# Kernel optimization log

Hardware: AMD Instinct MI355X
Metric: run time of the kernel (lower is better)

The kernel has to match this reference:

```python
import jax, jax.numpy as jnp
import numpy as np

N_HEAD = 16


def setup_inputs() -> dict:
    key = jax.random.key(0)
    k1, k2, k3 = jax.random.split(key, 3)
    B, T, C = 2, 2048, 1024
    x = jax.random.normal(k1, (B, T, C), dtype=jnp.float32)
    attention_mask = jnp.zeros((B, 1, 1, T), dtype=jnp.float32)
    W_attn = jax.random.normal(k2, (C, 3 * C), dtype=jnp.float32) * 0.02
    b_attn = jnp.zeros((3 * C,), dtype=jnp.float32)
    W_proj = jax.random.normal(k3, (C, C), dtype=jnp.float32) * 0.02
    b_proj = jnp.zeros((C,), dtype=jnp.float32)
    return {"x": x, "attention_mask": attention_mask, "W_attn": W_attn,
            "b_attn": b_attn, "W_proj": W_proj, "b_proj": b_proj}


def reference(x, attention_mask, W_attn, b_attn, W_proj, b_proj):
    B, T, C = x.shape
    H = N_HEAD
    d = C // H
    qkv = x @ W_attn + b_attn                      # [B, T, 3C]
    q, k, v = jnp.split(qkv, 3, axis=-1)
    q = q.reshape(B, T, H, d).transpose(0, 2, 1, 3)  # [B, H, T, d]
    k = k.reshape(B, T, H, d).transpose(0, 2, 1, 3)
    v = v.reshape(B, T, H, d).transpose(0, 2, 1, 3)
    att = jnp.einsum('bhtd,bhsd->bhts', q, k) * (1.0 / np.sqrt(d))
    causal = jnp.tril(jnp.ones((T, T), dtype=bool))
    att = jnp.where(causal[None, None], att, jnp.float32(-10000.0))
    att = att + attention_mask                     # additive broadcast mask
    att = jax.nn.softmax(att, axis=-1)             # dropout p=0.0 -> identity
    y = jnp.einsum('bhts,bhsd->bhtd', att, v)      # [B, H, T, d]
    y = y.transpose(0, 2, 1, 3).reshape(B, T, C)
    return y @ W_proj + b_proj
```

## Files before the change

kernel.cpp:

```cpp
#include <hip/hip_runtime.h>
#include <hip/hip_bf16.h>
#include <stdint.h>

#define BATCH 2
#define TT 2048
#define CC 1024
#define NH 16
#define HD 64

typedef __attribute__((ext_vector_type(8))) short short8;
typedef __attribute__((ext_vector_type(4))) short sh4;
typedef __attribute__((ext_vector_type(4))) float f32x4;
typedef __attribute__((ext_vector_type(2))) unsigned uint2v;

#define MFMA16 __builtin_amdgcn_mfma_f32_16x16x32_bf16

#define LOG2E 1.4426950408889634f

#if defined(__has_builtin)
#if __has_builtin(__builtin_amdgcn_exp2f)
#define EXP2(x) __builtin_amdgcn_exp2f(x)
#else
#define EXP2(x) __expf((x) * 0.6931471805599453f)
#endif
#else
#define EXP2(x) __expf((x) * 0.6931471805599453f)
#endif

__device__ __forceinline__ short f2bf(float f) {
  union { float f; unsigned u; } x;
  x.f = f;
  unsigned r = x.u + 0x7FFFu + ((x.u >> 16) & 1u);
  return (short)(r >> 16);
}

__device__ __forceinline__ void transpose_cast_tile(
    const float* __restrict__ W, short* __restrict__ Wt, int K, int N,
    int n0, int k0, int tid) {
  __shared__ __align__(16) float Ls[64][68];
  {
    const int r = tid >> 4, c4 = (tid & 15) * 4;
#pragma unroll
    for (int p = 0; p < 4; ++p) {
      const float4 v = *reinterpret_cast<const float4*>(
          &W[(size_t)(k0 + r + p * 16) * N + n0 + c4]);
      *reinterpret_cast<float4*>(&Ls[r + p * 16][c4]) = v;
    }
  }
  __syncthreads();
  {
    const int n = tid >> 2;
    const int kk0 = (tid & 3) * 16;
#pragma unroll
    for (int half = 0; half < 2; ++half) {
      short8 o;
#pragma unroll
      for (int t = 0; t < 8; ++t) o[t] = f2bf(Ls[kk0 + half * 8 + t][n]);
      *reinterpret_cast<short8*>(&Wt[(size_t)(n0 + n) * K + k0 + kk0 + half * 8]) = o;
    }
  }
}

__global__ __launch_bounds__(256) void prep_fused(
    const float* __restrict__ x, short* __restrict__ xb,
    const float* __restrict__ W_attn, short* __restrict__ wat,
    const float* __restrict__ W_proj, short* __restrict__ wpt) {
  const int blk = blockIdx.x;
  const int tid = threadIdx.x;
  if (blk < 2048) {
    const int i = (blk * 256 + tid) * 8;
    const float4 a = *reinterpret_cast<const float4*>(&x[i]);
    const float4 b = *reinterpret_cast<const float4*>(&x[i + 4]);
    short8 o;
    o[0] = f2bf(a.x); o[1] = f2bf(a.y); o[2] = f2bf(a.z); o[3] = f2bf(a.w);
    o[4] = f2bf(b.x); o[5] = f2bf(b.y); o[6] = f2bf(b.z); o[7] = f2bf(b.w);
    *reinterpret_cast<short8*>(&xb[i]) = o;
  } else if (blk < 2816) {
    const int b2 = blk - 2048;
    transpose_cast_tile(W_attn, wat, CC, 3 * CC, (b2 % 48) * 64,
                        (b2 / 48) * 64, tid);
  } else {
    const int b3 = blk - 2816;
    transpose_cast_tile(W_proj, wpt, CC, CC, (b3 % 16) * 64, (b3 / 16) * 64,
                        tid);
  }
}

__global__ __launch_bounds__(256) void transpose_v(
    const short* __restrict__ qkv, short* __restrict__ vT) {
  __shared__ __align__(16) short Ls[64][72];
  const int s0 = blockIdx.x * 64;
  const int bh = blockIdx.y, b = bh >> 4, h = bh & 15;
  const int tid = threadIdx.x;
  const int r = tid >> 3, c = (tid & 7) * 8;
#pragma unroll
  for (int p = 0; p < 2; ++p) {
    *reinterpret_cast<short8*>(&Ls[r + p * 32][c]) =
        *reinterpret_cast<const short8*>(
            &qkv[(size_t)(b * TT + s0 + r + p * 32) * (3 * CC) + 2 * CC +
                 h * HD + c]);
  }
  __syncthreads();
  const int d = tid >> 2, ss = (tid & 3) * 16;
  short8 o0, o1;
#pragma unroll
  for (int t = 0; t < 8; ++t) { o0[t] = Ls[ss + t][d]; o1[t] = Ls[ss + 8 + t][d]; }
  short* dst = &vT[((size_t)(bh * HD + d)) * TT + s0 + ss];
  *reinterpret_cast<short8*>(dst) = o0;
  *reinterpret_cast<short8*>(dst + 8) = o1;
}

template <bool OUT_BF16>
__global__ __launch_bounds__(256) void gemm_bt_mfma(
    const short* __restrict__ A, const short* __restrict__ Bt,
    const float* __restrict__ bias, void* __restrict__ C, int M, int N, int K,
    int QS) {
  __shared__ __align__(16) short As[2 * 128 * 32];
  __shared__ __align__(16) short Bs[2 * 128 * 32];
  const int tid = threadIdx.x;
  const int w = tid >> 6, lane = tid & 63;
  const int quad = lane >> 4, l15 = lane & 15;
  const int m0 = blockIdx.y * 128, n0 = blockIdx.x * 128;
  const int wm = (w >> 1) * 64, wn = (w & 1) * 64;

  f32x4 acc[4][4] = {};
  const int row16 = lane >> 2;
  const int c4 = (lane & 3) * 8;

  for (int k0 = 0; k0 < K; k0 += 64) {
    __syncthreads();
#pragma unroll
    for (int p = 0; p < 2; ++p) {
      const int rbase = __builtin_amdgcn_readfirstlane((w * 2 + p) * 16);
#pragma unroll
      for (int kh = 0; kh < 2; ++kh) {
        const short* ga = &A[(size_t)(m0 + rbase + row16) * K + k0 + kh * 32 + c4];
        const short* gb = &Bt[(size_t)(n0 + rbase + row16) * K + k0 + kh * 32 + c4];
        __builtin_amdgcn_global_load_lds(
            (const __attribute__((address_space(1))) void*)ga,
            (__attribute__((address_space(3))) void*)&As[kh * 4096 + rbase * 32],
            16, 0, 0);
        __builtin_amdgcn_global_load_lds(
            (const __attribute__((address_space(1))) void*)gb,
            (__attribute__((address_space(3))) void*)&Bs[kh * 4096 + rbase * 32],
            16, 0, 0);
      }
    }
    __syncthreads();

    short8 af[2][4], bfr[2][4];
#pragma unroll
    for (int kh = 0; kh < 2; ++kh) {
#pragma unroll
      for (int i = 0; i < 4; ++i)
        af[kh][i] = *reinterpret_cast<const short8*>(
            &As[kh * 4096 + (wm + i * 16 + l15) * 32 + quad * 8]);
#pragma unroll
      for (int j = 0; j < 4; ++j)
        bfr[kh][j] = *reinterpret_cast<const short8*>(
            &Bs[kh * 4096 + (wn + j * 16 + l15) * 32 + quad * 8]);
    }
#pragma unroll
    for (int kh = 0; kh < 2; ++kh)
#pragma unroll
      for (int i = 0; i < 4; ++i)
#pragma unroll
        for (int j = 0; j < 4; ++j)
          acc[i][j] = MFMA16(af[kh][i], bfr[kh][j], acc[i][j], 0, 0, 0);
  }

#pragma unroll
  for (int i = 0; i < 4; ++i) {
#pragma unroll
    for (int r = 0; r < 4; ++r) {
      const int row = m0 + wm + i * 16 + quad * 4 + r;
#pragma unroll
      for (int j = 0; j < 4; ++j) {
        const int col = n0 + wn + j * 16 + l15;
        float v = acc[i][j][r] + bias[col];
        if (col < QS) v *= 0.18033688011112042f;
        if (OUT_BF16)
          ((short*)C)[(size_t)row * N + col] = f2bf(v);
        else
          ((float*)C)[(size_t)row * N + col] = v;
      }
    }
  }
}

#define PST 72
__global__ __launch_bounds__(256) void attn_mfma8(
    const short* __restrict__ qkv, const short* __restrict__ vT,
    const float* __restrict__ mask, short* __restrict__ y) {
  __shared__ __align__(16) short Ks[2][64 * PST];
  __shared__ __align__(16) short Vs[2][64 * PST];
  __shared__ __align__(16) short Ps[64 * PST];
  const int tid = threadIdx.x;
  const int w = tid >> 6, lane = tid & 63;
  const int quad = lane >> 4, l15 = lane & 15;
  const int bh = blockIdx.y, b = bh >> 4, h = bh & 15;
  const int px = blockIdx.x;
  const int qh = 31 - px;
  const int nth = qh + 1;
  const int ntot = nth + px + 1;
  const int RS = 3 * CC;

  int qt = qh;
  int qrow0 = qt * 64 + w * 16;

  short8 qf0, qf1;
  {
    const size_t qrow = (size_t)(b * TT + qrow0 + l15) * RS + h * HD + quad * 8;
    qf0 = *reinterpret_cast<const short8*>(&qkv[qrow]);
    qf1 = *reinterpret_cast<const short8*>(&qkv[qrow + 32]);
  }

  float l_run = 0.f;
  f32x4 o_acc[4] = {};

  const int sr = tid >> 3, sc = (tid & 7) * 8;
  const short* kbase = qkv + (size_t)(b * TT + sr) * RS + CC + h * HD + sc;
  const short* vbase = vT + (size_t)(bh * HD + sr) * TT + sc;
  const float* mptr = mask + b * TT + quad * 4;
  short* psrow = &Ps[(w * 16 + l15) * PST];
  const int kfo0 = quad * 8, kfo1 = 32 + quad * 8;

  short8 kpre0 = *reinterpret_cast<const short8*>(kbase);
  short8 kpre1 = *reinterpret_cast<const short8*>(kbase + (size_t)32 * RS);
  short8 vpre0 = *reinterpret_cast<const short8*>(vbase);
  short8 vpre1 = *reinterpret_cast<const short8*>(vbase + 32 * TT);

  for (int it = 0; it < ntot; ++it) {
    const int kt = (it < nth) ? it : it - nth;
    const int s0 = kt * 64;

    f32x4 mv[4];
#pragma unroll
    for (int j = 0; j < 4; ++j)
      mv[j] = *reinterpret_cast<const f32x4*>(&mptr[s0 + j * 16]);

    if (it == nth) {
#pragma unroll
      for (int r = 0; r < 4; ++r) {
        const float lr = __shfl(l_run, quad * 4 + r, 64);
        const float inv = 1.0f / lr;
        const size_t row = (size_t)(b * TT + qrow0 + quad * 4 + r);
#pragma unroll
        for (int t = 0; t < 4; ++t)
          y[row * CC + h * HD + t * 16 + l15] = f2bf(o_acc[t][r] * inv);
      }
      qt = px;
      qrow0 = qt * 64 + w * 16;
      const size_t qrow = (size_t)(b * TT + qrow0 + l15) * RS + h * HD + quad * 8;
      qf0 = *reinterpret_cast<const short8*>(&qkv[qrow]);
      qf1 = *reinterpret_cast<const short8*>(&qkv[qrow + 32]);
      l_run = 0.f;
#pragma unroll
      for (int t = 0; t < 4; ++t) o_acc[t] = f32x4{0.f, 0.f, 0.f, 0.f};
    }

    const int cur = it & 1;
    *reinterpret_cast<short8*>(&Ks[cur][sr * PST + sc]) = kpre0;
    *reinterpret_cast<short8*>(&Ks[cur][(sr + 32) * PST + sc]) = kpre1;
    *reinterpret_cast<short8*>(&Vs[cur][sr * PST + sc]) = vpre0;
    *reinterpret_cast<short8*>(&Vs[cur][(sr + 32) * PST + sc]) = vpre1;
    __syncthreads();

    if (it + 1 < ntot) {
      const int ktn = (it + 1 == nth) ? 0 : kt + 1;
      const short* kp = kbase + (size_t)ktn * 64 * RS;
      const short* vp = vbase + ktn * 64;
      kpre0 = *reinterpret_cast<const short8*>(kp);
      kpre1 = *reinterpret_cast<const short8*>(kp + (size_t)32 * RS);
      vpre0 = *reinterpret_cast<const short8*>(vp);
      vpre1 = *reinterpret_cast<const short8*>(vp + 32 * TT);
    }

    f32x4 sa[4] = {};
#pragma unroll
    for (int j = 0; j < 4; ++j) {
      const short8 kf0 = *reinterpret_cast<const short8*>(
          &Ks[cur][(j * 16 + l15) * PST + kfo0]);
      const short8 kf1 = *reinterpret_cast<const short8*>(
          &Ks[cur][(j * 16 + l15) * PST + kfo1]);
      sa[j] = MFMA16(kf0, qf0, sa[j], 0, 0, 0);
      sa[j] = MFMA16(kf1, qf1, sa[j], 0, 0, 0);
    }

    float rs = 0.f;
    const bool boundary = (kt == qt);
    const int qg = qrow0 + l15;
#pragma unroll
    for (int j = 0; j < 4; ++j) {
      float pv[4];
#pragma unroll
      for (int r = 0; r < 4; ++r) {
        float v = __builtin_fmaf(mv[j][r], LOG2E, sa[j][r]);
        if (boundary) {
          const int sg = s0 + j * 16 + quad * 4 + r;
          if (sg > qg) v = -10000.0f;
        }
        pv[r] = EXP2(v);
      }
      union { __hip_bfloat162 h2[2]; uint2v u; } pk;
      pk.h2[0] = __float22bfloat162_rn(make_float2(pv[0], pv[1]));
      pk.h2[1] = __float22bfloat162_rn(make_float2(pv[2], pv[3]));
      *reinterpret_cast<uint2v*>(&psrow[j * 16 + quad * 4]) = pk.u;
      rs += (pv[0] + pv[1]) + (pv[2] + pv[3]);
    }
    rs += __shfl_xor(rs, 16, 64);
    rs += __shfl_xor(rs, 32, 64);
    l_run += rs;

    const short8 pf0 = *reinterpret_cast<const short8*>(&psrow[kfo0]);
    const short8 pf1 = *reinterpret_cast<const short8*>(&psrow[kfo1]);
#pragma unroll
    for (int t = 0; t < 4; ++t) {
      const short8 vf0 = *reinterpret_cast<const short8*>(
          &Vs[cur][(t * 16 + l15) * PST + kfo0]);
      const short8 vf1 = *reinterpret_cast<const short8*>(
          &Vs[cur][(t * 16 + l15) * PST + kfo1]);
      o_acc[t] = MFMA16(pf0, vf0, o_acc[t], 0, 0, 0);
      o_acc[t] = MFMA16(pf1, vf1, o_acc[t], 0, 0, 0);
    }
  }

#pragma unroll
  for (int r = 0; r < 4; ++r) {
    const float lr = __shfl(l_run, quad * 4 + r, 64);
    const float inv = 1.0f / lr;
    const size_t row = (size_t)(b * TT + qrow0 + quad * 4 + r);
#pragma unroll
    for (int t = 0; t < 4; ++t)
      y[row * CC + h * HD + t * 16 + l15] = f2bf(o_acc[t][r] * inv);
  }
}

extern "C" void kernel_launch(void* const* d_in, const int* in_sizes, int n_in,
                              void* d_out, int out_size, void* d_ws,
                              size_t ws_size, hipStream_t stream) {
  const float* x = (const float*)d_in[0];
  const float* attn_mask = (const float*)d_in[1];
  const float* W_attn = (const float*)d_in[2];
  const float* b_attn = (const float*)d_in[3];
  const float* W_proj = (const float*)d_in[4];
  const float* b_proj = (const float*)d_in[5];
  float* out = (float*)d_out;

  const int M = BATCH * TT;

  short* xb = (short*)d_ws;
  short* wat = xb + (size_t)M * CC;
  short* wpt = wat + (size_t)(3 * CC) * CC;
  short* qkvb = wpt + (size_t)CC * CC;
  short* yb = qkvb + (size_t)M * 3 * CC;
  short* vTb = yb + (size_t)M * CC;

  prep_fused<<<3072, 256, 0, stream>>>(x, xb, W_attn, wat, W_proj, wpt);

  gemm_bt_mfma<true><<<dim3((3 * CC) / 128, M / 128), 256, 0, stream>>>(
      xb, wat, b_attn, qkvb, M, 3 * CC, CC, CC);

  transpose_v<<<dim3(TT / 64, BATCH * NH), 256, 0, stream>>>(qkvb, vTb);

  attn_mfma8<<<dim3(16, BATCH * NH), 256, 0, stream>>>(
      qkvb, vTb, attn_mask, yb);

  gemm_bt_mfma<false><<<dim3(CC / 128, M / 128), 256, 0, stream>>>(
      yb, wpt, b_proj, out, M, CC, CC, 0);
}
```

Measured before the change: 202.9 us.

## Fuse all stages into one persistent cooperative kernel with grid syncs

Replaces the five separate kernel launches (prep, QKV GEMM, V transpose, attention, output GEMM) with a single cooperative persistent kernel. Each block statically partitions the work units of each phase and separates the phases with grid.sync(), sharing one dynamic-sized static shared buffer. This removes launch overhead and inter-kernel gaps, but adds grid-wide barrier cost, forces a uniform grid size that may be tuned poorly for each phase (attention only has 512 units and is causally imbalanced), and the larger shared buffer may lower occupancy.

```diff
diff --git a/kernel.cpp b/kernel.cpp
--- a/kernel.cpp
+++ b/kernel.cpp
@@ -1,5 +1,6 @@
 #include <hip/hip_runtime.h>
 #include <hip/hip_bf16.h>
+#include <hip/hip_cooperative_groups.h>
 #include <stdint.h>
 
 #define BATCH 2
@@ -7,14 +8,15 @@
 #define CC 1024
 #define NH 16
 #define HD 64
+#define PST 72
+
+namespace cg = cooperative_groups;
 
 typedef __attribute__((ext_vector_type(8))) short short8;
-typedef __attribute__((ext_vector_type(4))) short sh4;
 typedef __attribute__((ext_vector_type(4))) float f32x4;
 typedef __attribute__((ext_vector_type(2))) unsigned uint2v;
 
 #define MFMA16 __builtin_amdgcn_mfma_f32_16x16x32_bf16
-
 #define LOG2E 1.4426950408889634f
 
 #if defined(__has_builtin)
@@ -34,10 +36,24 @@
   return (short)(r >> 16);
 }
 
+
+__device__ __forceinline__ void xcast_unit(const float* __restrict__ x,
+                                           short* __restrict__ xb, int u,
+                                           int tid) {
+  const int i = (u * 256 + tid) * 8;
+  const float4 a = *reinterpret_cast<const float4*>(&x[i]);
+  const float4 b = *reinterpret_cast<const float4*>(&x[i + 4]);
+  short8 o;
+  o[0] = f2bf(a.x); o[1] = f2bf(a.y); o[2] = f2bf(a.z); o[3] = f2bf(a.w);
+  o[4] = f2bf(b.x); o[5] = f2bf(b.y); o[6] = f2bf(b.z); o[7] = f2bf(b.w);
+  *reinterpret_cast<short8*>(&xb[i]) = o;
+}
+
 __device__ __forceinline__ void transpose_cast_tile(
     const float* __restrict__ W, short* __restrict__ Wt, int K, int N,
-    int n0, int k0, int tid) {
-  __shared__ __align__(16) float Ls[64][68];
+    int n0, int k0, int tid, char* SMEM) {
+  float (*Ls)[68] = (float (*)[68])SMEM;
+  __syncthreads();
   {
     const int r = tid >> 4, c4 = (tid & 15) * 4;
 #pragma unroll
@@ -61,38 +77,14 @@
   }
 }
 
-__global__ __launch_bounds__(256) void prep_fused(
-    const float* __restrict__ x, short* __restrict__ xb,
-    const float* __restrict__ W_attn, short* __restrict__ wat,
-    const float* __restrict__ W_proj, short* __restrict__ wpt) {
-  const int blk = blockIdx.x;
-  const int tid = threadIdx.x;
-  if (blk < 2048) {
-    const int i = (blk * 256 + tid) * 8;
-    const float4 a = *reinterpret_cast<const float4*>(&x[i]);
-    const float4 b = *reinterpret_cast<const float4*>(&x[i + 4]);
-    short8 o;
-    o[0] = f2bf(a.x); o[1] = f2bf(a.y); o[2] = f2bf(a.z); o[3] = f2bf(a.w);
-    o[4] = f2bf(b.x); o[5] = f2bf(b.y); o[6] = f2bf(b.z); o[7] = f2bf(b.w);
-    *reinterpret_cast<short8*>(&xb[i]) = o;
-  } else if (blk < 2816) {
-    const int b2 = blk - 2048;
-    transpose_cast_tile(W_attn, wat, CC, 3 * CC, (b2 % 48) * 64,
-                        (b2 / 48) * 64, tid);
-  } else {
-    const int b3 = blk - 2816;
-    transpose_cast_tile(W_proj, wpt, CC, CC, (b3 % 16) * 64, (b3 / 16) * 64,
-                        tid);
-  }
-}
-
-__global__ __launch_bounds__(256) void transpose_v(
-    const short* __restrict__ qkv, short* __restrict__ vT) {
-  __shared__ __align__(16) short Ls[64][72];
-  const int s0 = blockIdx.x * 64;
-  const int bh = blockIdx.y, b = bh >> 4, h = bh & 15;
-  const int tid = threadIdx.x;
+__device__ __forceinline__ void tv_unit(const short* __restrict__ qkv,
+                                        short* __restrict__ vT, int u, int tid,
+                                        char* SMEM) {
+  short (*Ls)[72] = (short (*)[72])SMEM;
+  const int s0 = (u & 31) * 64;
+  const int bh = u >> 5, b = bh >> 4, h = bh & 15;
   const int r = tid >> 3, c = (tid & 7) * 8;
+  __syncthreads();
 #pragma unroll
   for (int p = 0; p < 2; ++p) {
     *reinterpret_cast<short8*>(&Ls[r + p * 32][c]) =
@@ -111,16 +103,15 @@
 }
 
 template <bool OUT_BF16>
-__global__ __launch_bounds__(256) void gemm_bt_mfma(
-    const short* __restrict__ A, const short* __restrict__ Bt,
-    const float* __restrict__ bias, void* __restrict__ C, int M, int N, int K,
-    int QS) {
-  __shared__ __align__(16) short As[2 * 128 * 32];
-  __shared__ __align__(16) short Bs[2 * 128 * 32];
-  const int tid = threadIdx.x;
+__device__ void gemm_tile(const short* __restrict__ A,
+                          const short* __restrict__ Bt,
+                          const float* __restrict__ bias, void* __restrict__ C,
+                          int N, int K, int QS, int m0, int n0, int tid,
+                          char* SMEM) {
+  short* As = (short*)SMEM;
+  short* Bs = (short*)(SMEM + 16384);
   const int w = tid >> 6, lane = tid & 63;
   const int quad = lane >> 4, l15 = lane & 15;
-  const int m0 = blockIdx.y * 128, n0 = blockIdx.x * 128;
   const int wm = (w >> 1) * 64, wn = (w & 1) * 64;
 
   f32x4 acc[4][4] = {};
@@ -188,22 +179,23 @@
   }
 }
 
-#define PST 72
-__global__ __launch_bounds__(256) void attn_mfma8(
-    const short* __restrict__ qkv, const short* __restrict__ vT,
-    const float* __restrict__ mask, short* __restrict__ y) {
-  __shared__ __align__(16) short Ks[2][64 * PST];
-  __shared__ __align__(16) short Vs[2][64 * PST];
-  __shared__ __align__(16) short Ps[64 * PST];
-  const int tid = threadIdx.x;
+__device__ void attn_unit(const short* __restrict__ qkv,
+                          const short* __restrict__ vT,
+                          const float* __restrict__ mask,
+                          short* __restrict__ y, int px, int bh, int tid,
+                          char* SMEM) {
+  short* Ks = (short*)SMEM;
+  short* Vs = (short*)(SMEM + 18432);
+  short* Ps = (short*)(SMEM + 36864);
   const int w = tid >> 6, lane = tid & 63;
   const int quad = lane >> 4, l15 = lane & 15;
-  const int bh = blockIdx.y, b = bh >> 4, h = bh & 15;
-  const int px = blockIdx.x;
+  const int b = bh >> 4, h = bh & 15;
   const int qh = 31 - px;
   const int nth = qh + 1;
   const int ntot = nth + px + 1;
   const int RS = 3 * CC;
+
+  __syncthreads();
 
   int qt = qh;
   int qrow0 = qt * 64 + w * 16;
@@ -260,10 +252,12 @@
     }
 
     const int cur = it & 1;
-    *reinterpret_cast<short8*>(&Ks[cur][sr * PST + sc]) = kpre0;
-    *reinterpret_cast<short8*>(&Ks[cur][(sr + 32) * PST + sc]) = kpre1;
-    *reinterpret_cast<short8*>(&Vs[cur][sr * PST + sc]) = vpre0;
-    *reinterpret_cast<short8*>(&Vs[cur][(sr + 32) * PST + sc]) = vpre1;
+    short* Kc = Ks + cur * (64 * PST);
+    short* Vc = Vs + cur * (64 * PST);
+    *reinterpret_cast<short8*>(&Kc[sr * PST + sc]) = kpre0;
+    *reinterpret_cast<short8*>(&Kc[(sr + 32) * PST + sc]) = kpre1;
+    *reinterpret_cast<short8*>(&Vc[sr * PST + sc]) = vpre0;
+    *reinterpret_cast<short8*>(&Vc[(sr + 32) * PST + sc]) = vpre1;
     __syncthreads();
 
     if (it + 1 < ntot) {
@@ -280,9 +274,9 @@
 #pragma unroll
     for (int j = 0; j < 4; ++j) {
       const short8 kf0 = *reinterpret_cast<const short8*>(
-          &Ks[cur][(j * 16 + l15) * PST + kfo0]);
+          &Kc[(j * 16 + l15) * PST + kfo0]);
       const short8 kf1 = *reinterpret_cast<const short8*>(
-          &Ks[cur][(j * 16 + l15) * PST + kfo1]);
+          &Kc[(j * 16 + l15) * PST + kfo1]);
       sa[j] = MFMA16(kf0, qf0, sa[j], 0, 0, 0);
       sa[j] = MFMA16(kf1, qf1, sa[j], 0, 0, 0);
     }
@@ -317,9 +311,9 @@
 #pragma unroll
     for (int t = 0; t < 4; ++t) {
       const short8 vf0 = *reinterpret_cast<const short8*>(
-          &Vs[cur][(t * 16 + l15) * PST + kfo0]);
+          &Vc[(t * 16 + l15) * PST + kfo0]);
       const short8 vf1 = *reinterpret_cast<const short8*>(
-          &Vs[cur][(t * 16 + l15) * PST + kfo1]);
+          &Vc[(t * 16 + l15) * PST + kfo1]);
       o_acc[t] = MFMA16(pf0, vf0, o_acc[t], 0, 0, 0);
       o_acc[t] = MFMA16(pf1, vf1, o_acc[t], 0, 0, 0);
     }
@@ -333,6 +327,72 @@
 #pragma unroll
     for (int t = 0; t < 4; ++t)
       y[row * CC + h * HD + t * 16 + l15] = f2bf(o_acc[t][r] * inv);
+  }
+}
+
+__global__ __launch_bounds__(256) void fused_all(
+    const float* __restrict__ x, short* __restrict__ xb,
+    const float* __restrict__ W_attn, short* __restrict__ wat,
+    const float* __restrict__ W_proj, short* __restrict__ wpt,
+    const float* __restrict__ b_attn, short* __restrict__ qkvb,
+    short* __restrict__ vTb, const float* __restrict__ mask,
+    short* __restrict__ yb, const float* __restrict__ b_proj,
+    float* __restrict__ out) {
+  __shared__ __align__(16) char SMEM[46080];
+  cg::grid_group grid = cg::this_grid();
+  const int tid = threadIdx.x;
+  const int bid = blockIdx.x;
+  const int nb = gridDim.x;
+
+  {
+    const int u0 = (int)((long)bid * 3072 / nb);
+    const int u1 = (int)((long)(bid + 1) * 3072 / nb);
+    for (int u = u0; u < u1; ++u) {
+      if (u < 2048) {
+        xcast_unit(x, xb, u, tid);
+      } else if (u < 2816) {
+        const int b2 = u - 2048;
+        transpose_cast_tile(W_attn, wat, CC, 3 * CC, (b2 % 48) * 64,
+                            (b2 / 48) * 64, tid, SMEM);
+      } else {
+        const int b3 = u - 2816;
+        transpose_cast_tile(W_proj, wpt, CC, CC, (b3 % 16) * 64,
+                            (b3 / 16) * 64, tid, SMEM);
+      }
+    }
+  }
+  grid.sync();
+
+  {
+    const int t0 = (int)((long)bid * 768 / nb);
+    const int t1 = (int)((long)(bid + 1) * 768 / nb);
+    for (int t = t0; t < t1; ++t)
+      gemm_tile<true>(xb, wat, b_attn, qkvb, 3 * CC, CC, CC,
+                      (t / 24) * 128, (t % 24) * 128, tid, SMEM);
+  }
+  grid.sync();
+
+  {
+    const int u0 = (int)((long)bid * 1024 / nb);
+    const int u1 = (int)((long)(bid + 1) * 1024 / nb);
+    for (int u = u0; u < u1; ++u) tv_unit(qkvb, vTb, u, tid, SMEM);
+  }
+  grid.sync();
+
+  {
+    const int u0 = (int)((long)bid * 512 / nb);
+    const int u1 = (int)((long)(bid + 1) * 512 / nb);
+    for (int u = u0; u < u1; ++u)
+      attn_unit(qkvb, vTb, mask, yb, u & 15, u >> 4, tid, SMEM);
+  }
+  grid.sync();
+
+  {
+    const int t0 = (int)((long)bid * 256 / nb);
+    const int t1 = (int)((long)(bid + 1) * 256 / nb);
+    for (int t = t0; t < t1; ++t)
+      gemm_tile<false>(yb, wpt, b_proj, out, CC, CC, 0,
+                       (t / 8) * 128, (t % 8) * 128, tid, SMEM);
   }
 }
 
@@ -356,16 +416,23 @@
   short* yb = qkvb + (size_t)M * 3 * CC;
   short* vTb = yb + (size_t)M * CC;
 
-  prep_fused<<<3072, 256, 0, stream>>>(x, xb, W_attn, wat, W_proj, wpt);
-
-  gemm_bt_mfma<true><<<dim3((3 * CC) / 128, M / 128), 256, 0, stream>>>(
-      xb, wat, b_attn, qkvb, M, 3 * CC, CC, CC);
-
-  transpose_v<<<dim3(TT / 64, BATCH * NH), 256, 0, stream>>>(qkvb, vTb);
-
-  attn_mfma8<<<dim3(16, BATCH * NH), 256, 0, stream>>>(
-      qkvb, vTb, attn_mask, yb);
-
-  gemm_bt_mfma<false><<<dim3(CC / 128, M / 128), 256, 0, stream>>>(
-      yb, wpt, b_proj, out, M, CC, CC, 0);
-}
+  static int coop_grid = 0;
+  if (coop_grid == 0) {
+    int maxb = 0;
+    if (hipOccupancyMaxActiveBlocksPerMultiprocessor(
+            &maxb, (const void*)fused_all, 256, 0) != hipSuccess ||
+        maxb < 1)
+      maxb = 1;
+    long nb = (long)maxb * 256;
+    if (nb > 768) nb = 768;
+    coop_grid = (int)nb;
+  }
+
+  void* args[13] = {
+      (void*)&x,     (void*)&xb,     (void*)&W_attn, (void*)&wat,
+      (void*)&W_proj,(void*)&wpt,    (void*)&b_attn, (void*)&qkvb,
+      (void*)&vTb,   (void*)&attn_mask, (void*)&yb,  (void*)&b_proj,
+      (void*)&out};
+  hipLaunchCooperativeKernel((const void*)fused_all, dim3(coop_grid),
+                             dim3(256), args, 0, stream);
+}
```

Result: slower. 397.3 us (+95.8%).
